# Performance work log

Measured on AMD Instinct MI355X. Metric: run time of the kernel, lower is better.

The kernel has to match this reference:

```python
import jax, jax.numpy as jnp
import numpy as np

VOCAB = 100000
N_NODES = 200000
D = 128


def setup_inputs() -> dict:
    key = jax.random.key(0)
    k1, k2, k3, k4, k5, k6 = jax.random.split(key, 6)
    nodes = jax.random.randint(k1, (N_NODES,), 0, VOCAB, dtype=jnp.int64 if jax.config.jax_enable_x64 else jnp.int32).astype(jnp.int32)
    c2e_weight = jax.random.normal(k2, (VOCAB, D), dtype=jnp.float32)
    w1 = jax.random.normal(k3, (D, D), dtype=jnp.float32) * (1.0 / np.sqrt(D))
    b1 = jax.random.normal(k4, (D,), dtype=jnp.float32) * 0.01
    w2 = jax.random.normal(k5, (D, D), dtype=jnp.float32) * (1.0 / np.sqrt(D))
    b2 = jax.random.normal(k6, (D,), dtype=jnp.float32) * 0.01
    return {"nodes": nodes, "c2e_weight": c2e_weight, "w1": w1, "b1": b1, "w2": w2, "b2": b2}


def reference(nodes, c2e_weight, w1, b1, w2, b2):
    # Vectorized version of the per-node Python loop:
    #   ce = c2e.weight[node]; x = relu(w_r1(ce)); out = relu(w_r2(x))
    ce = c2e_weight[nodes]                         # [N, D] gather
    h = jax.nn.relu(ce @ w1.T + b1)                # [N, D]
    out = jax.nn.relu(h @ w2.T + b2)               # [N, D]
    return out
```

## Files before the change

kernel.cpp:

```cpp
#include <hip/hip_runtime.h>
#include <hip/hip_bf16.h>

#define D_DIM   128
#define MT      64
#define NBLOCKS 512
#define NTHR    512

typedef __attribute__((ext_vector_type(8))) short bf16x8;
typedef __attribute__((ext_vector_type(4))) float f32x4;

__device__ __forceinline__ unsigned short f2bf(float f) {
    return __builtin_bit_cast(unsigned short, __float2bfloat16(f));
}

__device__ __forceinline__ int sw_off(int row, int col) {
    return row * 128 + ((((col >> 3) ^ (row & 15)) << 3) | (col & 7));
}

__device__ __forceinline__ void stage_w(const float* __restrict__ w,
                                        unsigned short* __restrict__ sW, int t) {
    #pragma unroll
    for (int i = 0; i < 8; ++i) {
        const int idx4 = i * NTHR + t;
        const float4 v = ((const float4*)w)[idx4];
        const int row = idx4 >> 5;
        const int c4  = (idx4 & 31) * 4;
        ushort4 b;
        b.x = f2bf(v.x); b.y = f2bf(v.y); b.z = f2bf(v.z); b.w = f2bf(v.w);
        *(ushort4*)&sW[sw_off(row, c4)] = b;
    }
}

__global__ __launch_bounds__(NTHR, 2)
void ctx_encoder(const int* __restrict__ nodes,
                 const float* __restrict__ c2e,
                 const float* __restrict__ w1,
                 const float* __restrict__ b1,
                 const float* __restrict__ w2,
                 const float* __restrict__ b2,
                 float* __restrict__ out,
                 int N) {
    __shared__ unsigned short sW1[D_DIM * 128];
    __shared__ unsigned short sW2[D_DIM * 128];
    __shared__ unsigned short sX [MT    * 128];

    const int t    = threadIdx.x;
    const int lane = t & 63;
    const int wave = t >> 6;
    const int pair = wave >> 1;
    const int half = wave & 1;
    const int cl   = lane & 15;
    const int quad = lane >> 4;

    const int grow0 = t >> 3;
    const int gc    = t & 7;

    stage_w(w1, sW1, t);
    stage_w(w2, sW2, t);

    float bias1[4], bias2[4];
    #pragma unroll
    for (int c = 0; c < 4; ++c) {
        const int j = (half * 4 + c) * 16 + cl;
        bias1[c] = b1[j];
        bias2[c] = b2[j];
    }

    const int nTiles = (N + MT - 1) / MT;
    int tl = blockIdx.x;

    int r0 = tl * MT + grow0;  r0 = r0 < N ? r0 : N - 1;
    int idx_cur = nodes[r0];
    float4 g[4];
    {
        const float* rp = c2e + (size_t)idx_cur * D_DIM + gc * 4;
        #pragma unroll
        for (int i = 0; i < 4; ++i)
            g[i] = *(const float4*)(rp + i * 32);
    }
    int idx_nxt = 0;
    if (tl + NBLOCKS < nTiles) {
        int r1 = (tl + NBLOCKS) * MT + grow0;  r1 = r1 < N ? r1 : N - 1;
        idx_nxt = nodes[r1];
    }
    __syncthreads();

    while (tl < nTiles) {
        #pragma unroll
        for (int i = 0; i < 4; ++i) {
            ushort4 b;
            b.x = f2bf(g[i].x); b.y = f2bf(g[i].y);
            b.z = f2bf(g[i].z); b.w = f2bf(g[i].w);
            *(ushort4*)&sX[sw_off(grow0, gc * 4 + i * 32)] = b;
        }
        __syncthreads();

        bf16x8 aF[4];
        #pragma unroll
        for (int ks = 0; ks < 4; ++ks)
            aF[ks] = *(const bf16x8*)&sX[sw_off(pair * 16 + cl, ks * 32 + quad * 8)];

        const int tn = tl + NBLOCKS;
        if (tn < nTiles) {
            const float* rp = c2e + (size_t)idx_nxt * D_DIM + gc * 4;
            #pragma unroll
            for (int i = 0; i < 4; ++i)
                g[i] = *(const float4*)(rp + i * 32);
            if (tn + NBLOCKS < nTiles) {
                int rn = (tn + NBLOCKS) * MT + grow0;  rn = rn < N ? rn : N - 1;
                idx_nxt = nodes[rn];
            }
        }
        __syncthreads();

        #pragma unroll
        for (int c = 0; c < 4; ++c) {
            const int ct = half * 4 + c;
            bf16x8 bF[4];
            #pragma unroll
            for (int ks = 0; ks < 4; ++ks)
                bF[ks] = *(const bf16x8*)&sW1[sw_off(ct * 16 + cl, ks * 32 + quad * 8)];
            f32x4 acc = {0.f, 0.f, 0.f, 0.f};
            #pragma unroll
            for (int ks = 0; ks < 4; ++ks)
                acc = __builtin_amdgcn_mfma_f32_16x16x32_bf16(aF[ks], bF[ks], acc, 0, 0, 0);
            const int j = ct * 16 + cl;
            #pragma unroll
            for (int r = 0; r < 4; ++r) {
                float h = acc[r] + bias1[c];
                h = h > 0.f ? h : 0.f;
                sX[sw_off(pair * 16 + quad * 4 + r, j)] = f2bf(h);
            }
        }
        __syncthreads();

        bf16x8 hF[4];
        #pragma unroll
        for (int ks = 0; ks < 4; ++ks)
            hF[ks] = *(const bf16x8*)&sX[sw_off(pair * 16 + cl, ks * 32 + quad * 8)];
        __syncthreads();

        const size_t obase = (size_t)tl * MT;
        #pragma unroll
        for (int c = 0; c < 4; ++c) {
            const int ct = half * 4 + c;
            bf16x8 bF[4];
            #pragma unroll
            for (int ks = 0; ks < 4; ++ks)
                bF[ks] = *(const bf16x8*)&sW2[sw_off(ct * 16 + cl, ks * 32 + quad * 8)];
            f32x4 acc = {0.f, 0.f, 0.f, 0.f};
            #pragma unroll
            for (int ks = 0; ks < 4; ++ks)
                acc = __builtin_amdgcn_mfma_f32_16x16x32_bf16(hF[ks], bF[ks], acc, 0, 0, 0);
            const int j = ct * 16 + cl;
            #pragma unroll
            for (int r = 0; r < 4; ++r) {
                float o = acc[r] + bias2[c];
                o = o > 0.f ? o : 0.f;
                const long grow = (long)(obase + pair * 16 + quad * 4 + r);
                if (grow < N)
                    out[(size_t)grow * D_DIM + j] = o;
            }
        }

        tl += NBLOCKS;
    }
}

extern "C" void kernel_launch(void* const* d_in, const int* in_sizes, int n_in,
                              void* d_out, int out_size, void* d_ws, size_t ws_size,
                              hipStream_t stream) {
    const int*   nodes = (const int*)d_in[0];
    const float* c2e   = (const float*)d_in[1];
    const float* w1    = (const float*)d_in[2];
    const float* b1    = (const float*)d_in[3];
    const float* w2    = (const float*)d_in[4];
    const float* b2    = (const float*)d_in[5];
    float* out = (float*)d_out;
    const int N = in_sizes[0];

    ctx_encoder<<<dim3(NBLOCKS), dim3(NTHR), 0, stream>>>(nodes, c2e, w1, b1, w2, b2, out, N);
}
```

Measured before the change: 163.7 us.

## Hold weight fragments in registers and shrink tiles to cut LDS and barriers

Each wave now keeps its bf16 fragments of W1 and W2 in registers for its two output column tiles instead of staging both weights in shared memory. LDS shrinks to two small 32-row buffers for the gathered input and the hidden activations. Tiles drop to 32 rows, blocks to 256 threads with more blocks and a higher occupancy hint, and two barriers per iteration are removed because separate buffers replace the shared sX reuse. Output stores become nontemporal. The trade-off is higher register pressure from the resident weight fragments, and every block redundantly reads the weights from global memory.

```diff
diff --git a/kernel.cpp b/kernel.cpp
--- a/kernel.cpp
+++ b/kernel.cpp
@@ -2,9 +2,9 @@
 #include <hip/hip_bf16.h>
 
 #define D_DIM   128
-#define MT      64
-#define NBLOCKS 512
-#define NTHR    512
+#define MT      32
+#define NBLOCKS 768
+#define NTHR    256
 
 typedef __attribute__((ext_vector_type(8))) short bf16x8;
 typedef __attribute__((ext_vector_type(4))) float f32x4;
@@ -17,21 +17,18 @@
     return row * 128 + ((((col >> 3) ^ (row & 15)) << 3) | (col & 7));
 }
 
-__device__ __forceinline__ void stage_w(const float* __restrict__ w,
-                                        unsigned short* __restrict__ sW, int t) {
-    #pragma unroll
-    for (int i = 0; i < 8; ++i) {
-        const int idx4 = i * NTHR + t;
-        const float4 v = ((const float4*)w)[idx4];
-        const int row = idx4 >> 5;
-        const int c4  = (idx4 & 31) * 4;
-        ushort4 b;
-        b.x = f2bf(v.x); b.y = f2bf(v.y); b.z = f2bf(v.z); b.w = f2bf(v.w);
-        *(ushort4*)&sW[sw_off(row, c4)] = b;
-    }
+__device__ __forceinline__ bf16x8 load_wfrag(const float* __restrict__ w, int j, int kb) {
+    const float4 lo = *(const float4*)(w + j * D_DIM + kb);
+    const float4 hi = *(const float4*)(w + j * D_DIM + kb + 4);
+    bf16x8 r;
+    r[0] = (short)f2bf(lo.x); r[1] = (short)f2bf(lo.y);
+    r[2] = (short)f2bf(lo.z); r[3] = (short)f2bf(lo.w);
+    r[4] = (short)f2bf(hi.x); r[5] = (short)f2bf(hi.y);
+    r[6] = (short)f2bf(hi.z); r[7] = (short)f2bf(hi.w);
+    return r;
 }
 
-__global__ __launch_bounds__(NTHR, 2)
+__global__ __launch_bounds__(NTHR, 3)
 void ctx_encoder(const int* __restrict__ nodes,
                  const float* __restrict__ c2e,
                  const float* __restrict__ w1,
@@ -40,30 +37,31 @@
                  const float* __restrict__ b2,
                  float* __restrict__ out,
                  int N) {
-    __shared__ unsigned short sW1[D_DIM * 128];
-    __shared__ unsigned short sW2[D_DIM * 128];
-    __shared__ unsigned short sX [MT    * 128];
+    __shared__ unsigned short sA[MT * 128];
+    __shared__ unsigned short sH[MT * 128];
 
     const int t    = threadIdx.x;
     const int lane = t & 63;
     const int wave = t >> 6;
-    const int pair = wave >> 1;
-    const int half = wave & 1;
     const int cl   = lane & 15;
     const int quad = lane >> 4;
 
     const int grow0 = t >> 3;
     const int gc    = t & 7;
 
-    stage_w(w1, sW1, t);
-    stage_w(w2, sW2, t);
-
-    float bias1[4], bias2[4];
+    bf16x8 wB1[2][4], wB2[2][4];
+    float bias1[2], bias2[2];
     #pragma unroll
-    for (int c = 0; c < 4; ++c) {
-        const int j = (half * 4 + c) * 16 + cl;
+    for (int c = 0; c < 2; ++c) {
+        const int j = (wave * 2 + c) * 16 + cl;
         bias1[c] = b1[j];
         bias2[c] = b2[j];
+        #pragma unroll
+        for (int ks = 0; ks < 4; ++ks) {
+            const int kb = ks * 32 + quad * 8;
+            wB1[c][ks] = load_wfrag(w1, j, kb);
+            wB2[c][ks] = load_wfrag(w2, j, kb);
+        }
     }
 
     const int nTiles = (N + MT - 1) / MT;
@@ -83,7 +81,6 @@
         int r1 = (tl + NBLOCKS) * MT + grow0;  r1 = r1 < N ? r1 : N - 1;
         idx_nxt = nodes[r1];
     }
-    __syncthreads();
 
     while (tl < nTiles) {
         #pragma unroll
@@ -91,14 +88,16 @@
             ushort4 b;
             b.x = f2bf(g[i].x); b.y = f2bf(g[i].y);
             b.z = f2bf(g[i].z); b.w = f2bf(g[i].w);
-            *(ushort4*)&sX[sw_off(grow0, gc * 4 + i * 32)] = b;
+            *(ushort4*)&sA[sw_off(grow0, gc * 4 + i * 32)] = b;
         }
         __syncthreads();
 
-        bf16x8 aF[4];
+        bf16x8 aF[2][4];
         #pragma unroll
-        for (int ks = 0; ks < 4; ++ks)
-            aF[ks] = *(const bf16x8*)&sX[sw_off(pair * 16 + cl, ks * 32 + quad * 8)];
+        for (int m = 0; m < 2; ++m)
+            #pragma unroll
+            for (int ks = 0; ks < 4; ++ks)
+                aF[m][ks] = *(const bf16x8*)&sA[sw_off(m * 16 + cl, ks * 32 + quad * 8)];
 
         const int tn = tl + NBLOCKS;
         if (tn < nTiles) {
@@ -111,55 +110,51 @@
                 idx_nxt = nodes[rn];
             }
         }
-        __syncthreads();
 
         #pragma unroll
-        for (int c = 0; c < 4; ++c) {
-            const int ct = half * 4 + c;
-            bf16x8 bF[4];
+        for (int m = 0; m < 2; ++m) {
             #pragma unroll
-            for (int ks = 0; ks < 4; ++ks)
-                bF[ks] = *(const bf16x8*)&sW1[sw_off(ct * 16 + cl, ks * 32 + quad * 8)];
-            f32x4 acc = {0.f, 0.f, 0.f, 0.f};
-            #pragma unroll
-            for (int ks = 0; ks < 4; ++ks)
-                acc = __builtin_amdgcn_mfma_f32_16x16x32_bf16(aF[ks], bF[ks], acc, 0, 0, 0);
-            const int j = ct * 16 + cl;
-            #pragma unroll
-            for (int r = 0; r < 4; ++r) {
-                float h = acc[r] + bias1[c];
-                h = h > 0.f ? h : 0.f;
-                sX[sw_off(pair * 16 + quad * 4 + r, j)] = f2bf(h);
+            for (int c = 0; c < 2; ++c) {
+                f32x4 acc = {0.f, 0.f, 0.f, 0.f};
+                #pragma unroll
+                for (int ks = 0; ks < 4; ++ks)
+                    acc = __builtin_amdgcn_mfma_f32_16x16x32_bf16(aF[m][ks], wB1[c][ks], acc, 0, 0, 0);
+                const int j = (wave * 2 + c) * 16 + cl;
+                #pragma unroll
+                for (int r = 0; r < 4; ++r) {
+                    float h = acc[r] + bias1[c];
+                    h = h > 0.f ? h : 0.f;
+                    sH[sw_off(m * 16 + quad * 4 + r, j)] = f2bf(h);
+                }
             }
         }
         __syncthreads();
 
-        bf16x8 hF[4];
+        bf16x8 hF[2][4];
         #pragma unroll
-        for (int ks = 0; ks < 4; ++ks)
-            hF[ks] = *(const bf16x8*)&sX[sw_off(pair * 16 + cl, ks * 32 + quad * 8)];
-        __syncthreads();
+        for (int m = 0; m < 2; ++m)
+            #pragma unroll
+            for (int ks = 0; ks < 4; ++ks)
+                hF[m][ks] = *(const bf16x8*)&sH[sw_off(m * 16 + cl, ks * 32 + quad * 8)];
 
         const size_t obase = (size_t)tl * MT;
         #pragma unroll
-        for (int c = 0; c < 4; ++c) {
-            const int ct = half * 4 + c;
-            bf16x8 bF[4];
+        for (int m = 0; m < 2; ++m) {
             #pragma unroll
-            for (int ks = 0; ks < 4; ++ks)
-                bF[ks] = *(const bf16x8*)&sW2[sw_off(ct * 16 + cl, ks * 32 + quad * 8)];
-            f32x4 acc = {0.f, 0.f, 0.f, 0.f};
-            #pragma unroll
-            for (int ks = 0; ks < 4; ++ks)
-                acc = __builtin_amdgcn_mfma_f32_16x16x32_bf16(hF[ks], bF[ks], acc, 0, 0, 0);
-            const int j = ct * 16 + cl;
-            #pragma unroll
-            for (int r = 0; r < 4; ++r) {
-                float o = acc[r] + bias2[c];
-                o = o > 0.f ? o : 0.f;
-                const long grow = (long)(obase + pair * 16 + quad * 4 + r);
-                if (grow < N)
-                    out[(size_t)grow * D_DIM + j] = o;
+            for (int c = 0; c < 2; ++c) {
+                f32x4 acc = {0.f, 0.f, 0.f, 0.f};
+                #pragma unroll
+                for (int ks = 0; ks < 4; ++ks)
+                    acc = __builtin_amdgcn_mfma_f32_16x16x32_bf16(hF[m][ks], wB2[c][ks], acc, 0, 0, 0);
+                const int j = (wave * 2 + c) * 16 + cl;
+                #pragma unroll
+                for (int r = 0; r < 4; ++r) {
+                    float o = acc[r] + bias2[c];
+                    o = o > 0.f ? o : 0.f;
+                    const long grow = (long)(obase + m * 16 + quad * 4 + r);
+                    if (grow < N)
+                        __builtin_nontemporal_store(o, &out[(size_t)grow * D_DIM + j]);
+                }
             }
         }
 
```

Result: slower. 181.3 us (+10.8%).
